# Kernel tuning notes

Hardware: AMD Instinct MI355X
Metric: run time of the kernel (lower is better)

Reference implementation:

```python
import jax, jax.numpy as jnp
import numpy as np

OUT_H, OUT_W = 384, 384


def _affine_grid(theta, out_h, out_w):
    # theta: [B, 2, 3]. Normalized target grid in [-1, 1], homogeneous coords.
    ys = jnp.linspace(-1.0, 1.0, out_h)
    xs = jnp.linspace(-1.0, 1.0, out_w)
    gy, gx = jnp.meshgrid(ys, xs, indexing='ij')            # [out_h, out_w]
    ones = jnp.ones_like(gx)
    grid = jnp.stack([gx.ravel(), gy.ravel(), ones.ravel()])  # [3, out_h*out_w]
    src = jnp.einsum('bij,jn->bin', theta, grid)              # [B, 2, N]
    return src[:, 0, :], src[:, 1, :]                         # x, y in [-1,1]


def _bilinear_sample(img, x, y):
    # img: [B, Hi, Wi, C]; x, y: [B, N] normalized coords in [-1, 1]
    B, Hi, Wi, C = img.shape
    x = (x + 1.0) * (Wi - 1) * 0.5
    y = (y + 1.0) * (Hi - 1) * 0.5
    x0f = jnp.floor(x)
    y0f = jnp.floor(y)
    x0 = jnp.clip(x0f.astype(jnp.int32), 0, Wi - 1)
    x1 = jnp.clip(x0f.astype(jnp.int32) + 1, 0, Wi - 1)
    y0 = jnp.clip(y0f.astype(jnp.int32), 0, Hi - 1)
    y1 = jnp.clip(y0f.astype(jnp.int32) + 1, 0, Hi - 1)
    # interpolation weights from unclipped fractional parts
    wx1 = x - x0f
    wx0 = 1.0 - wx1
    wy1 = y - y0f
    wy0 = 1.0 - wy1
    flat = img.reshape(B, Hi * Wi, C)

    def gather(yy, xx):
        idx = yy * Wi + xx                                   # [B, N]
        return jnp.take_along_axis(flat, idx[:, :, None], axis=1)  # [B, N, C]

    out = (gather(y0, x0) * (wy0 * wx0)[:, :, None]
           + gather(y0, x1) * (wy0 * wx1)[:, :, None]
           + gather(y1, x0) * (wy1 * wx0)[:, :, None]
           + gather(y1, x1) * (wy1 * wx1)[:, :, None])
    return out


def reference(X, W_loc, b_loc):
    # Localization net: global average pool over HW, then linear -> theta [B, 6]
    B, Hi, Wi, C = X.shape
    feat = X.mean(axis=(1, 2))                               # [B, C]
    theta = (feat @ W_loc + b_loc).reshape(B, 2, 3)
    x, y = _affine_grid(theta, OUT_H, OUT_W)                 # [B, N] each
    out = _bilinear_sample(X, x, y)                          # [B, N, C]
    return out.reshape(B, OUT_H, OUT_W, C)


def setup_inputs() -> dict:
    key = jax.random.key(0)
    k1, k2, k3 = jax.random.split(key, 3)
    X = jax.random.normal(k1, (16, 384, 384, 32), dtype=jnp.float32)
    # small-scale locnet weights so theta stays near a mild transform
    W_loc = jax.random.normal(k2, (32, 6), dtype=jnp.float32) * 0.1
    b_loc = jnp.array([1.0, 0.0, 0.0, 0.0, 1.0, 0.0], dtype=jnp.float32) \
            + jax.random.normal(k3, (6,), dtype=jnp.float32) * 0.05
    return {"X": X, "W_loc": W_loc, "b_loc": b_loc}
```

## Files before the change

kernel.cpp:

```cpp
#include <hip/hip_runtime.h>

#define BATCH 16
#define HI 384
#define WI 384
#define CH 32
#define OUT_H 384
#define OUT_W 384
#define HW (HI * WI)
#define NBLK 128
#define NPIX (BATCH * OUT_H * OUT_W)
#define TILE_W 8
#define TILE_H 4
#define TILES_X (OUT_W / TILE_W)
#define TILES_Y (OUT_H / TILE_H)
#define TILES_PER_IMG (TILES_X * TILES_Y)
#define SAMP_BLOCKS (BATCH * TILES_PER_IMG)

typedef float f32x4 __attribute__((ext_vector_type(4)));

__global__ __launch_bounds__(256) void k_partial_sums(
    const float* __restrict__ X, float* __restrict__ partials) {
  const int blk = blockIdx.x;
  const int b = blk / NBLK;
  const int sub = blk % NBLK;
  const int t = threadIdx.x;
  const int c4 = t & 7;
  const int poff = t >> 3;
  const int ppb = HW / NBLK;
  const int p0 = sub * ppb;

  const f32x4* base = (const f32x4*)(X + (size_t)b * HW * CH);
  f32x4 acc = {0.f, 0.f, 0.f, 0.f};
#pragma unroll 4
  for (int p = p0 + poff; p < p0 + ppb; p += 32) {
    acc += base[(size_t)p * 8 + c4];
  }

  __shared__ f32x4 sh[256];
  sh[t] = acc;
  __syncthreads();
  if (t < 8) {
    f32x4 s = {0.f, 0.f, 0.f, 0.f};
    for (int i = 0; i < 32; ++i) s += sh[i * 8 + t];
    ((f32x4*)(partials + (size_t)blk * CH))[t] = s;
  }
}

__global__ __launch_bounds__(512) void k_theta(
    const float* __restrict__ partials, const float* __restrict__ Wl,
    const float* __restrict__ bl, float* __restrict__ theta) {
  __shared__ float feat[BATCH * CH];
  const int t = threadIdx.x;
  {
    const int b = t >> 5, c = t & 31;
    float s = 0.f;
#pragma unroll 8
    for (int i = 0; i < NBLK; ++i)
      s += partials[((size_t)b * NBLK + i) * CH + c];
    feat[t] = s * (1.0f / (float)HW);
  }
  __syncthreads();
  if (t < BATCH * 6) {
    const int b = t / 6, j = t % 6;
    float s = bl[j];
    for (int c = 0; c < CH; ++c) s += feat[b * CH + c] * Wl[c * 6 + j];
    theta[t] = s;
  }
}

__global__ __launch_bounds__(256) void k_sample(
    const float* __restrict__ X, const float* __restrict__ theta,
    float* __restrict__ out) {
  const int q = SAMP_BLOCKS >> 3;
  const int bid = blockIdx.x;
  const int blk = (bid & 7) * q + (bid >> 3);

  const int b = blk / TILES_PER_IMG;
  const int tl = blk % TILES_PER_IMG;
  const int tx = tl / TILES_Y;
  const int ty = tl % TILES_Y;

  const int t = threadIdx.x;
  const int c4 = t & 7;
  const int px = t >> 3;
  const int col = px & 7;
  const int row = px >> 3;

  const int ox = tx * TILE_W + col;
  const int oy = ty * TILE_H + row;

  const float* th = theta + b * 6;
  const float gx = fmaf((float)ox, 2.0f / (float)(OUT_W - 1), -1.0f);
  const float gy = fmaf((float)oy, 2.0f / (float)(OUT_H - 1), -1.0f);
  const float sx = th[0] * gx + th[1] * gy + th[2];
  const float sy = th[3] * gx + th[4] * gy + th[5];
  const float x = (sx + 1.0f) * 0.5f * (float)(WI - 1);
  const float y = (sy + 1.0f) * 0.5f * (float)(HI - 1);

  const float x0f = floorf(x), y0f = floorf(y);
  const float wx1 = x - x0f, wx0 = 1.0f - wx1;
  const float wy1 = y - y0f, wy0 = 1.0f - wy1;
  const int x0 = min(max((int)x0f, 0), WI - 1);
  const int x1 = min(max((int)x0f + 1, 0), WI - 1);
  const int y0 = min(max((int)y0f, 0), HI - 1);
  const int y1 = min(max((int)y0f + 1, 0), HI - 1);

  const f32x4* img = (const f32x4*)(X + (size_t)b * HW * CH);
  const f32x4 g00 = img[((size_t)y0 * WI + x0) * 8 + c4];
  const f32x4 g01 = img[((size_t)y0 * WI + x1) * 8 + c4];
  const f32x4 g10 = img[((size_t)y1 * WI + x0) * 8 + c4];
  const f32x4 g11 = img[((size_t)y1 * WI + x1) * 8 + c4];

  const float w00 = wy0 * wx0, w01 = wy0 * wx1;
  const float w10 = wy1 * wx0, w11 = wy1 * wx1;

  const f32x4 r = g00 * w00 + g01 * w01 + g10 * w10 + g11 * w11;

  const size_t n = (size_t)b * (OUT_H * OUT_W) + (size_t)oy * OUT_W + ox;
  __builtin_nontemporal_store(r, (f32x4*)out + n * 8 + c4);
}

extern "C" void kernel_launch(void* const* d_in, const int* in_sizes, int n_in,
                              void* d_out, int out_size, void* d_ws,
                              size_t ws_size, hipStream_t stream) {
  const float* X = (const float*)d_in[0];
  const float* Wl = (const float*)d_in[1];
  const float* bl = (const float*)d_in[2];
  float* out = (float*)d_out;

  float* partials = (float*)d_ws;
  float* theta = partials + (size_t)BATCH * NBLK * CH;

  k_partial_sums<<<BATCH * NBLK, 256, 0, stream>>>(X, partials);
  k_theta<<<1, 512, 0, stream>>>(partials, Wl, bl, theta);
  k_sample<<<SAMP_BLOCKS, 256, 0, stream>>>(X, theta, out);
}
```

Baseline: 173.5 us.

## Stage source footprint in LDS and process larger output tiles per block

Each block now covers a 12x8 output tile over three passes. It computes the bounding box of the source pixels from the tile corners and, when that box fits within 224 pixels, loads it into shared memory once. The bilinear gathers then read from LDS instead of issuing four global loads per pixel, with a fallback to direct global gathers for large footprints. This cuts redundant global and L2 traffic from overlapping neighbour reads, at the cost of a staging loop, a block barrier, LDS usage and fewer blocks.

```diff
diff --git a/kernel.cpp b/kernel.cpp
--- a/kernel.cpp
+++ b/kernel.cpp
@@ -8,13 +8,17 @@
 #define OUT_W 384
 #define HW (HI * WI)
 #define NBLK 128
-#define NPIX (BATCH * OUT_H * OUT_W)
-#define TILE_W 8
-#define TILE_H 4
+
+#define TILE_W 12
+#define TILE_H 8
+#define PASSES 3
 #define TILES_X (OUT_W / TILE_W)
 #define TILES_Y (OUT_H / TILE_H)
 #define TILES_PER_IMG (TILES_X * TILES_Y)
 #define SAMP_BLOCKS (BATCH * TILES_PER_IMG)
+
+#define MAXPX 224
+#define PXSTRIDE (MAXPX + 2)
 
 typedef float f32x4 __attribute__((ext_vector_type(4)));
 
@@ -68,6 +72,17 @@
   }
 }
 
+__device__ __forceinline__ void map_xy(float th0, float th1, float th2,
+                                       float th3, float th4, float th5,
+                                       int ox, int oy, float& x, float& y) {
+  const float gx = fmaf((float)ox, 2.0f / (float)(OUT_W - 1), -1.0f);
+  const float gy = fmaf((float)oy, 2.0f / (float)(OUT_H - 1), -1.0f);
+  const float sx = th0 * gx + th1 * gy + th2;
+  const float sy = th3 * gx + th4 * gy + th5;
+  x = (sx + 1.0f) * 0.5f * (float)(WI - 1);
+  y = (sy + 1.0f) * 0.5f * (float)(HI - 1);
+}
+
 __global__ __launch_bounds__(256) void k_sample(
     const float* __restrict__ X, const float* __restrict__ theta,
     float* __restrict__ out) {
@@ -79,45 +94,89 @@
   const int tl = blk % TILES_PER_IMG;
   const int tx = tl / TILES_Y;
   const int ty = tl % TILES_Y;
+  const int ox0 = tx * TILE_W;
+  const int oy0 = ty * TILE_H;
+
+  const float th0 = theta[b * 6 + 0], th1 = theta[b * 6 + 1],
+              th2 = theta[b * 6 + 2], th3 = theta[b * 6 + 3],
+              th4 = theta[b * 6 + 4], th5 = theta[b * 6 + 5];
+
+  float xa, ya, xb, yb, xc, yc, xd, yd;
+  map_xy(th0, th1, th2, th3, th4, th5, ox0, oy0, xa, ya);
+  map_xy(th0, th1, th2, th3, th4, th5, ox0 + TILE_W - 1, oy0, xb, yb);
+  map_xy(th0, th1, th2, th3, th4, th5, ox0, oy0 + TILE_H - 1, xc, yc);
+  map_xy(th0, th1, th2, th3, th4, th5, ox0 + TILE_W - 1, oy0 + TILE_H - 1, xd, yd);
+  const float xminf = fminf(fminf(xa, xb), fminf(xc, xd));
+  const float xmaxf = fmaxf(fmaxf(xa, xb), fmaxf(xc, xd));
+  const float yminf = fminf(fminf(ya, yb), fminf(yc, yd));
+  const float ymaxf = fmaxf(fmaxf(ya, yb), fmaxf(yc, yd));
+  const int ixmin = min(max((int)floorf(xminf) - 1, 0), WI - 1);
+  const int ixmax = min(max((int)floorf(xmaxf) + 2, 0), WI - 1);
+  const int iymin = min(max((int)floorf(yminf) - 1, 0), HI - 1);
+  const int iymax = min(max((int)floorf(ymaxf) + 2, 0), HI - 1);
+  const int W = ixmax - ixmin + 1;
+  const int H = iymax - iymin + 1;
+  const bool staged = (W * H <= MAXPX);
+
+  __shared__ f32x4 lds[8 * PXSTRIDE];
 
   const int t = threadIdx.x;
   const int c4 = t & 7;
-  const int px = t >> 3;
-  const int col = px & 7;
-  const int row = px >> 3;
+  const int lane_px = t >> 3;
+  const f32x4* img = (const f32x4*)(X + (size_t)b * HW * CH);
 
-  const int ox = tx * TILE_W + col;
-  const int oy = ty * TILE_H + row;
+  if (staged) {
+    for (int r = 0; r < H; ++r) {
+      for (int cc = lane_px; cc < W; cc += 32) {
+        lds[c4 * PXSTRIDE + r * W + cc] =
+            img[((size_t)(iymin + r) * WI + (ixmin + cc)) * 8 + c4];
+      }
+    }
+    __syncthreads();
+  }
 
-  const float* th = theta + b * 6;
-  const float gx = fmaf((float)ox, 2.0f / (float)(OUT_W - 1), -1.0f);
-  const float gy = fmaf((float)oy, 2.0f / (float)(OUT_H - 1), -1.0f);
-  const float sx = th[0] * gx + th[1] * gy + th[2];
-  const float sy = th[3] * gx + th[4] * gy + th[5];
-  const float x = (sx + 1.0f) * 0.5f * (float)(WI - 1);
-  const float y = (sy + 1.0f) * 0.5f * (float)(HI - 1);
+  const size_t obase = (size_t)b * (OUT_H * OUT_W);
+#pragma unroll
+  for (int p = 0; p < PASSES; ++p) {
+    const int pi = p * 32 + lane_px;
+    const int col = pi % TILE_W;
+    const int row = pi / TILE_W;
+    const int ox = ox0 + col;
+    const int oy = oy0 + row;
 
-  const float x0f = floorf(x), y0f = floorf(y);
-  const float wx1 = x - x0f, wx0 = 1.0f - wx1;
-  const float wy1 = y - y0f, wy0 = 1.0f - wy1;
-  const int x0 = min(max((int)x0f, 0), WI - 1);
-  const int x1 = min(max((int)x0f + 1, 0), WI - 1);
-  const int y0 = min(max((int)y0f, 0), HI - 1);
-  const int y1 = min(max((int)y0f + 1, 0), HI - 1);
+    float x, y;
+    map_xy(th0, th1, th2, th3, th4, th5, ox, oy, x, y);
 
-  const f32x4* img = (const f32x4*)(X + (size_t)b * HW * CH);
-  const f32x4 g00 = img[((size_t)y0 * WI + x0) * 8 + c4];
-  const f32x4 g01 = img[((size_t)y0 * WI + x1) * 8 + c4];
-  const f32x4 g10 = img[((size_t)y1 * WI + x0) * 8 + c4];
-  const f32x4 g11 = img[((size_t)y1 * WI + x1) * 8 + c4];
+    const float x0f = floorf(x), y0f = floorf(y);
+    const float wx1 = x - x0f, wx0 = 1.0f - wx1;
+    const float wy1 = y - y0f, wy0 = 1.0f - wy1;
+    const int x0 = min(max((int)x0f, 0), WI - 1);
+    const int x1 = min(max((int)x0f + 1, 0), WI - 1);
+    const int y0 = min(max((int)y0f, 0), HI - 1);
+    const int y1 = min(max((int)y0f + 1, 0), HI - 1);
 
-  const float w00 = wy0 * wx0, w01 = wy0 * wx1;
-  const float w10 = wy1 * wx0, w11 = wy1 * wx1;
+    f32x4 g00, g01, g10, g11;
+    if (staged) {
+      const int r0 = (y0 - iymin) * W - ixmin;
+      const int r1 = (y1 - iymin) * W - ixmin;
+      g00 = lds[c4 * PXSTRIDE + r0 + x0];
+      g01 = lds[c4 * PXSTRIDE + r0 + x1];
+      g10 = lds[c4 * PXSTRIDE + r1 + x0];
+      g11 = lds[c4 * PXSTRIDE + r1 + x1];
+    } else {
+      g00 = img[((size_t)y0 * WI + x0) * 8 + c4];
+      g01 = img[((size_t)y0 * WI + x1) * 8 + c4];
+      g10 = img[((size_t)y1 * WI + x0) * 8 + c4];
+      g11 = img[((size_t)y1 * WI + x1) * 8 + c4];
+    }
 
-  const f32x4 r = g00 * w00 + g01 * w01 + g10 * w10 + g11 * w11;
+    const float w00 = wy0 * wx0, w01 = wy0 * wx1;
+    const float w10 = wy1 * wx0, w11 = wy1 * wx1;
+    const f32x4 r = g00 * w00 + g01 * w01 + g10 * w10 + g11 * w11;
 
-  const size_t n = (size_t)b * (OUT_H * OUT_W) + (size_t)oy * OUT_W + ox;
-  __builtin_nontemporal_store(r, (f32x4*)out + n * 8 + c4);
+    const size_t n = (obase + (size_t)oy * OUT_W + ox) * 8 + c4;
+    __builtin_nontemporal_store(r, (f32x4*)out + n);
+  }
 }
 
 extern "C" void kernel_launch(void* const* d_in, const int* in_sizes, int n_in,
```

After: 239.7 us. 38.2% more time.
